# Kernel optimization log

Hardware: AMD Instinct MI355X
Metric: run time of the kernel (lower is better)

The kernel has to match this reference:

```python
import jax, jax.numpy as jnp
import numpy as np

N, E, HID, H, D = 16000, 128000, 128, 8, 16
EPS = 1e-6
LN_EPS = 1e-5


def _ln(x, g, b):
    mu = x.mean(-1, keepdims=True)
    var = ((x - mu) ** 2).mean(-1, keepdims=True)
    return (x - mu) * jax.lax.rsqrt(var + LN_EPS) * g + b


def _phi(x):
    return jax.nn.elu(x) + 1.0


def setup_inputs() -> dict:
    key = jax.random.key(0)
    ks = jax.random.split(key, 16)
    w = lambda k, s: (jax.random.normal(k, s, jnp.float32) * 0.02)
    inp = {
        'x': jax.random.normal(ks[0], (N, HID), jnp.float32),
        'r': jax.random.normal(ks[1], (E, HID), jnp.float32),
        'edge_index': jax.random.randint(ks[2], (2, E), 0, N, jnp.int64),
        # layernorms
        'ln_x_g': jnp.ones((HID,)), 'ln_x_b': jnp.zeros((HID,)),
        'ln_r_g': jnp.ones((HID,)), 'ln_r_b': jnp.zeros((HID,)),
        'ln_post_g': jnp.ones((HID,)), 'ln_post_b': jnp.zeros((HID,)),
        'ln_ffpre_g': jnp.ones((HID,)), 'ln_ffpre_b': jnp.zeros((HID,)),
        'ln_ffpost_g': jnp.ones((HID,)), 'ln_ffpost_b': jnp.zeros((HID,)),
        # attention projections (stored [in, out]; y = x @ W)
        'Wq': w(ks[3], (HID, H * D)), 'Wk': w(ks[4], (HID, H * D)),
        'Wv': w(ks[5], (HID, H * D)),
        'Wkr': w(ks[6], (HID, H * D)), 'Wvr': w(ks[7], (HID, H * D)),
        'Wo': w(ks[8], (H * D, HID)),
        'Wg': w(ks[9], (2 * HID, HID)), 'bg': jnp.zeros((HID,)),
        'Ws': w(ks[10], (HID, HID)), 'bs': jnp.zeros((HID,)),
        # feed-forward
        'W1': w(ks[11], (HID, 4 * HID)), 'b1': jnp.zeros((4 * HID,)),
        'W2': w(ks[12], (4 * HID, HID)), 'b2': jnp.zeros((HID,)),
    }
    return inp


def reference(x, r, edge_index, ln_x_g, ln_x_b, ln_r_g, ln_r_b,
              ln_post_g, ln_post_b, ln_ffpre_g, ln_ffpre_b,
              ln_ffpost_g, ln_ffpost_b, Wq, Wk, Wv, Wkr, Wvr, Wo,
              Wg, bg, Ws, bs, W1, b1, W2, b2):
    n = x.shape[0]
    src, dst = edge_index[0], edge_index[1]
    xs = _ln(x, ln_x_g, ln_x_b)            # shared pre-norm (non-bipartite)
    rn = _ln(r, ln_r_g, ln_r_b)

    q = (xs @ Wq).reshape(n, H, D)
    k = (xs @ Wk).reshape(n, H, D)
    v = (xs @ Wv).reshape(n, H, D)
    k_e = k[src] + (rn @ Wkr).reshape(-1, H, D)   # [E,H,D]
    v_e = v[src] + (rn @ Wvr).reshape(-1, H, D)

    phi_q = _phi(q)                         # [N,H,D]
    phi_k = _phi(k_e)                       # [E,H,D]
    # per-edge outer product, scattered to destination nodes
    kv = phi_k[..., :, None] * v_e[..., None, :]          # [E,H,D,D]
    S = jax.ops.segment_sum(kv.reshape(-1, H * D * D), dst,
                            num_segments=n).reshape(n, H, D, D)
    Z = jax.ops.segment_sum(phi_k.reshape(-1, H * D), dst,
                            num_segments=n).reshape(n, H, D)

    num = jnp.einsum('nhd,nhdv->nhv', phi_q, S)
    den = jnp.maximum((phi_q * Z).sum(-1, keepdims=True), EPS)
    out = (num / den).reshape(n, H * D) @ Wo              # [N,HID]

    g = jax.nn.sigmoid(jnp.concatenate([out, xs], axis=-1) @ Wg + bg)
    attn = out + g * (xs @ Ws + bs - out)

    x_mid = x + _ln(attn, ln_post_g, ln_post_b)
    h = jax.nn.gelu(_ln(x_mid, ln_ffpre_g, ln_ffpre_b) @ W1 + b1,
                    approximate=False) @ W2 + b2
    return x_mid + _ln(h, ln_ffpost_g, ln_ffpost_b)
```

## Files before the change

kernel.cpp:

```cpp
#include <hip/hip_runtime.h>
#include <hip/hip_bf16.h>

#define NN 16000
#define NE 128000

typedef unsigned short u16;
typedef __attribute__((ext_vector_type(8))) short bf16x8;
typedef __attribute__((ext_vector_type(4))) float f32x4;

__device__ __forceinline__ float bf2f(u16 u) {
    unsigned int v = ((unsigned int)u) << 16;
    return __uint_as_float(v);
}
__device__ __forceinline__ u16 f2bf(float f) {
    unsigned int u = __float_as_uint(f);
    unsigned int r = u + 0x7FFF + ((u >> 16) & 1);
    return (u16)(r >> 16);
}
__device__ __forceinline__ float loadf(const void* p, size_t i, int bf) {
    return bf ? bf2f(((const u16*)p)[i]) : ((const float*)p)[i];
}

__global__ void dtype_detect_kernel(const u16* __restrict__ xw, int* __restrict__ flags)
{
    __shared__ int cnt[256];
    if (threadIdx.x == 0) flags[2] = 0;
    int c = 0;
    #pragma unroll
    for (int k = 0; k < 16; ++k) {
        unsigned int w = xw[threadIdx.x + k * 256];
        int e = (int)((w >> 7) & 0xFF);
        c += (e >= 100 && e <= 140) ? 1 : 0;
    }
    cnt[threadIdx.x] = c;
    __syncthreads();
    for (int s = 128; s > 0; s >>= 1) {
        if (threadIdx.x < s) cnt[threadIdx.x] += cnt[threadIdx.x + s];
        __syncthreads();
    }
    if (threadIdx.x == 0) flags[0] = (cnt[0] >= 3300) ? 1 : 0;
}

__global__ __launch_bounds__(256) void edetect_kernel(const int* __restrict__ ei,
                                                      int* __restrict__ flags)
{
    int t = blockIdx.x * 256 + threadIdx.x;
    int a = 0;
    #pragma unroll
    for (int j = 0; j < 4; ++j) a |= ei[2 * (t * 4 + j) + 1];
    for (int m = 1; m < 64; m <<= 1) a |= __shfl_xor(a, m, 64);
    if ((threadIdx.x & 63) == 0 && a) atomicOr(&flags[2], a);
}

__global__ void cvt_edges_kernel(const int* __restrict__ ei, const int* __restrict__ flags,
                                 int* __restrict__ out, int* __restrict__ hist)
{
    int i = blockIdx.x * 256 + threadIdx.x;
    if (i < NN) hist[i] = 0;
    if (i >= 2 * NE) return;
    int v = (flags[2] == 0) ? ei[2 * i] : ei[i];
    v = v < 0 ? 0 : (v >= NN ? NN - 1 : v);
    out[i] = v;
}

__global__ void hist_kernel(const int* __restrict__ e32, int* __restrict__ hist)
{
    int i = blockIdx.x * 256 + threadIdx.x;
    if (i < NE) atomicAdd(&hist[e32[NE + i]], 1);
}

__global__ __launch_bounds__(256) void scan_kernel(const int* __restrict__ hist,
                                                   int* __restrict__ offs,
                                                   int* __restrict__ cursor)
{
    __shared__ int wsum[4];
    __shared__ int carry_s;
    int tid = threadIdx.x, lane = tid & 63, w = tid >> 6;
    if (tid == 0) { carry_s = 0; offs[0] = 0; cursor[0] = 0; }
    __syncthreads();
    for (int c0 = 0; c0 < NN; c0 += 256) {
        int i = c0 + tid;
        int x = (i < NN) ? hist[i] : 0;
        #pragma unroll
        for (int o = 1; o < 64; o <<= 1) {
            int y = __shfl_up(x, o, 64);
            if (lane >= o) x += y;
        }
        if (lane == 63) wsum[w] = x;
        __syncthreads();
        if (tid == 0) {
            int s = 0;
            #pragma unroll
            for (int j = 0; j < 4; ++j) { int t2 = wsum[j]; wsum[j] = s; s += t2; }
        }
        __syncthreads();
        int incl = x + wsum[w] + carry_s;
        if (i < NN) { offs[i + 1] = incl; cursor[i + 1] = incl; }
        __syncthreads();
        if (tid == 255) carry_s = incl;
        __syncthreads();
    }
}

__global__ void scatter_kernel(const int* __restrict__ e32, int* __restrict__ cursor,
                               int* __restrict__ perm, int* __restrict__ ssrc,
                               int* __restrict__ sdst)
{
    int i = blockIdx.x * 256 + threadIdx.x;
    if (i >= NE) return;
    int d = e32[NE + i];
    int pos = atomicAdd(&cursor[d], 1);
    perm[pos] = i;
    ssrc[pos] = e32[i];
    sdst[pos] = d;
}

struct WDesc { const void* w; u16* wt; int K; int N; int tile0; };
struct WTArgs { WDesc d[10]; };
__global__ __launch_bounds__(256) void wtrans_kernel(WTArgs args, const int* __restrict__ flags)
{
    int b = blockIdx.x;
    int i = 0;
    while (i < 9 && b >= args.d[i + 1].tile0) ++i;
    WDesc de = args.d[i];
    int lt = b - de.tile0;
    int tn = de.N >> 5;
    int tk = lt / tn, tc = lt % tn;
    int bf = flags[0];
    int n = tc * 32 + (threadIdx.x & 31);
    int k = tk * 32 + ((threadIdx.x >> 5) << 2);
    u16* dp = de.wt + (size_t)n * de.K + k;
    #pragma unroll
    for (int j = 0; j < 4; ++j)
        dp[j] = f2bf(loadf(de.w, (size_t)(k + j) * de.N + n, bf));
}

__global__ __launch_bounds__(256) void ln_in_kernel(const void* __restrict__ X,
                                                    const void* __restrict__ gain,
                                                    const void* __restrict__ beta,
                                                    const int* __restrict__ flags,
                                                    u16* __restrict__ Y, int M)
{
    const int bf = flags[0];
    int row = blockIdx.x * 4 + (threadIdx.x >> 6);
    int lane = threadIdx.x & 63;
    if (row >= M) return;
    size_t base = (size_t)row * 128;
    float x0 = loadf(X, base + lane, bf);
    float x1 = loadf(X, base + lane + 64, bf);
    float s = x0 + x1, sq = x0 * x0 + x1 * x1;
    for (int m = 1; m < 64; m <<= 1) { s += __shfl_xor(s, m, 64); sq += __shfl_xor(sq, m, 64); }
    float mu = s * (1.0f / 128.0f);
    float var = sq * (1.0f / 128.0f) - mu * mu;
    float rs = rsqrtf(var + 1e-5f);
    Y[base + lane]      = f2bf((x0 - mu) * rs * loadf(gain, lane, bf)      + loadf(beta, lane, bf));
    Y[base + lane + 64] = f2bf((x1 - mu) * rs * loadf(gain, lane + 64, bf) + loadf(beta, lane + 64, bf));
}

__global__ __launch_bounds__(256) void mfma_gemm_kernel(
    const u16* __restrict__ A, const u16* __restrict__ Wt, int bstride,
    const void* __restrict__ bias, const int* __restrict__ flags,
    void* __restrict__ C, int M, int K, int Ncol, int act, int out_bf)
{
    int wave = threadIdx.x >> 6, lane = threadIdx.x & 63;
    int quad = lane >> 4, l15 = lane & 15;
    int m0 = blockIdx.y * 64 + wave * 16;
    int n0 = blockIdx.x * 64;
    f32x4 acc[4] = {};
    const u16* ap = A + (size_t)(m0 + l15) * K + quad * 8;
    const u16* bp = Wt + (size_t)(n0 + l15) * bstride + quad * 8;
    for (int k0 = 0; k0 < K; k0 += 32) {
        bf16x8 a = *(const bf16x8*)(ap + k0);
        #pragma unroll
        for (int t = 0; t < 4; ++t) {
            bf16x8 b = *(const bf16x8*)(bp + (size_t)(t * 16) * bstride + k0);
            acc[t] = __builtin_amdgcn_mfma_f32_16x16x32_bf16(a, b, acc[t], 0, 0, 0);
        }
    }
    const int bf = flags[0];
    #pragma unroll
    for (int t = 0; t < 4; ++t) {
        int col = n0 + t * 16 + l15;
        float bv = bias ? loadf(bias, col, bf) : 0.0f;
        #pragma unroll
        for (int rg = 0; rg < 4; ++rg) {
            int row = m0 + quad * 4 + rg;
            float v = acc[t][rg] + bv;
            if (act == 1 || (act == 3 && col < 128)) v = (v > 0.0f) ? v + 1.0f : expf(v);
            else if (act == 2) v = 0.5f * v * (1.0f + erff(v * 0.70710678118f));
            if (out_bf) ((u16*)C)[(size_t)row * Ncol + col] = f2bf(v);
            else        ((float*)C)[(size_t)row * Ncol + col] = v;
        }
    }
}

__global__ __launch_bounds__(256) void edge_proj_kernel(
    const void* __restrict__ r,
    const void* __restrict__ lng, const void* __restrict__ lnb,
    const u16* __restrict__ Wkrt, const u16* __restrict__ Wvrt,
    const int* __restrict__ perm, const int* __restrict__ ssrc,
    const int* __restrict__ sdst,
    const u16* __restrict__ qkv, const int* __restrict__ flags,
    float* __restrict__ p_arr, u16* __restrict__ ve_s)
{
    const int bf = flags[0];
    __shared__ float sg[128], sb[128];
    int tid = threadIdx.x;
    if (tid < 128) { sg[tid] = loadf(lng, tid, bf); sb[tid] = loadf(lnb, tid, bf); }
    __syncthreads();
    int wave = tid >> 6, lane = tid & 63;
    int quad = lane >> 4, l15 = lane & 15;
    int e0 = blockIdx.x * 32 + (wave >> 1) * 16;
    int c0 = (wave & 1) * 64;

    int rrow = perm[e0 + l15];
    float vbuf[32];
    float s = 0.f, sq = 0.f;
    size_t rbase = (size_t)rrow * 128;
    #pragma unroll
    for (int kc = 0; kc < 4; ++kc) {
        int cb = kc * 32 + quad * 8;
        if (bf) {
            ushort4 p0 = *(const ushort4*)((const u16*)r + rbase + cb);
            ushort4 p1 = *(const ushort4*)((const u16*)r + rbase + cb + 4);
            vbuf[kc*8+0]=bf2f(p0.x); vbuf[kc*8+1]=bf2f(p0.y); vbuf[kc*8+2]=bf2f(p0.z); vbuf[kc*8+3]=bf2f(p0.w);
            vbuf[kc*8+4]=bf2f(p1.x); vbuf[kc*8+5]=bf2f(p1.y); vbuf[kc*8+6]=bf2f(p1.z); vbuf[kc*8+7]=bf2f(p1.w);
        } else {
            float4 p0 = *(const float4*)((const float*)r + rbase + cb);
            float4 p1 = *(const float4*)((const float*)r + rbase + cb + 4);
            vbuf[kc*8+0]=p0.x; vbuf[kc*8+1]=p0.y; vbuf[kc*8+2]=p0.z; vbuf[kc*8+3]=p0.w;
            vbuf[kc*8+4]=p1.x; vbuf[kc*8+5]=p1.y; vbuf[kc*8+6]=p1.z; vbuf[kc*8+7]=p1.w;
        }
        #pragma unroll
        for (int j = 0; j < 8; ++j) { s += vbuf[kc*8+j]; sq += vbuf[kc*8+j]*vbuf[kc*8+j]; }
    }
    s += __shfl_xor(s, 16, 64); sq += __shfl_xor(sq, 16, 64);
    s += __shfl_xor(s, 32, 64); sq += __shfl_xor(sq, 32, 64);
    float mu = s * (1.0f / 128.0f);
    float var = sq * (1.0f / 128.0f) - mu * mu;
    float rsx = rsqrtf(var + 1e-5f);
    bf16x8 afr[4];
    #pragma unroll
    for (int kc = 0; kc < 4; ++kc) {
        bf16x8 a;
        #pragma unroll
        for (int j = 0; j < 8; ++j) {
            int col = kc * 32 + quad * 8 + j;
            a[j] = (short)f2bf((vbuf[kc*8+j] - mu) * rsx * sg[col] + sb[col]);
        }
        afr[kc] = a;
    }

    f32x4 acck[4] = {};
    f32x4 accv[4] = {};
    #pragma unroll
    for (int kc = 0; kc < 4; ++kc) {
        int k0 = kc * 32;
        #pragma unroll
        for (int t = 0; t < 4; ++t) {
            bf16x8 bk = *(const bf16x8*)(Wkrt + (size_t)(c0 + t*16 + l15) * 128 + k0 + quad * 8);
            bf16x8 bv = *(const bf16x8*)(Wvrt + (size_t)(c0 + t*16 + l15) * 128 + k0 + quad * 8);
            acck[t] = __builtin_amdgcn_mfma_f32_16x16x32_bf16(afr[kc], bk, acck[t], 0, 0, 0);
            accv[t] = __builtin_amdgcn_mfma_f32_16x16x32_bf16(afr[kc], bv, accv[t], 0, 0, 0);
        }
    }

    int se[4], de[4];
    #pragma unroll
    for (int rg = 0; rg < 4; ++rg) {
        int e = e0 + quad * 4 + rg;
        se[rg] = ssrc[e]; de[rg] = sdst[e];
    }
    #pragma unroll
    for (int t = 0; t < 4; ++t) {
        int col = c0 + t * 16 + l15;
        float p_[4];
        #pragma unroll
        for (int rg = 0; rg < 4; ++rg) {
            float kv = acck[t][rg] + bf2f(qkv[(size_t)se[rg] * 384 + 128 + col]);
            kv = (kv > 0.0f) ? kv + 1.0f : expf(kv);
            float pm = kv * bf2f(qkv[(size_t)de[rg] * 384 + col]);
            pm += __shfl_xor(pm, 1, 64);
            pm += __shfl_xor(pm, 2, 64);
            pm += __shfl_xor(pm, 4, 64);
            pm += __shfl_xor(pm, 8, 64);
            p_[rg] = pm;
        }
        if (l15 == 0) {
            #pragma unroll
            for (int rg = 0; rg < 4; ++rg)
                p_arr[(size_t)(e0 + quad * 4 + rg) * 8 + (c0 >> 4) + t] = p_[rg];
        }
        #pragma unroll
        for (int rg = 0; rg < 4; ++rg) {
            float vv = accv[t][rg] + bf2f(qkv[(size_t)se[rg] * 384 + 256 + col]);
            ve_s[(size_t)(e0 + quad * 4 + rg) * 128 + col] = f2bf(vv);
        }
    }
}

__global__ __launch_bounds__(256) void node_acc_kernel(
    const float* __restrict__ p_arr, const u16* __restrict__ ve_s,
    const int* __restrict__ offs, u16* __restrict__ att)
{
    int n = blockIdx.x * 4 + (threadIdx.x >> 6);
    int lane = threadIdx.x & 63;
    int beg = offs[n], end = offs[n + 1];
    int h0 = lane >> 4, h1 = 4 + h0;
    float n0 = 0.f, n1 = 0.f, d0 = 0.f, d1 = 0.f;
    for (int e = beg; e < end; ++e) {
        float p0 = p_arr[(size_t)e * 8 + h0];
        float p1 = p_arr[(size_t)e * 8 + h1];
        float v0 = bf2f(ve_s[(size_t)e * 128 + lane]);
        float v1 = bf2f(ve_s[(size_t)e * 128 + lane + 64]);
        n0 += p0 * v0; n1 += p1 * v1;
        d0 += p0; d1 += p1;
    }
    att[(size_t)n * 128 + lane]      = f2bf(n0 / fmaxf(d0, 1e-6f));
    att[(size_t)n * 128 + lane + 64] = f2bf(n1 / fmaxf(d1, 1e-6f));
}

__global__ __launch_bounds__(256) void gate_mega_kernel(
    const u16* __restrict__ att,
    const u16* __restrict__ Wo_t, const u16* __restrict__ Wg_t,
    const float* __restrict__ gxs, const float* __restrict__ sbuf,
    const void* __restrict__ x,
    const void* __restrict__ g_po, const void* __restrict__ b_po,
    const void* __restrict__ g_fp, const void* __restrict__ b_fp,
    const int* __restrict__ flags,
    float* __restrict__ xmid, u16* __restrict__ ffp)
{
    const int bf = flags[0];
    __shared__ float lds[4][16][132];
    __shared__ float sgpo[128], sbpo[128], sgfp[128], sbfp[128];
    int tid = threadIdx.x;
    if (tid < 128) {
        sgpo[tid] = loadf(g_po, tid, bf);
        sbpo[tid] = loadf(b_po, tid, bf);
        sgfp[tid] = loadf(g_fp, tid, bf);
        sbfp[tid] = loadf(b_fp, tid, bf);
    }
    __syncthreads();
    int wave = tid >> 6, lane = tid & 63;
    int quad = lane >> 4, l15 = lane & 15;
    int m0 = blockIdx.x * 64 + wave * 16;

    bf16x8 afr[4];
    #pragma unroll
    for (int kc = 0; kc < 4; ++kc)
        afr[kc] = *(const bf16x8*)(att + (size_t)(m0 + l15) * 128 + kc * 32 + quad * 8);

    f32x4 acco[8] = {};
    #pragma unroll
    for (int kc = 0; kc < 4; ++kc)
        #pragma unroll
        for (int t = 0; t < 8; ++t) {
            bf16x8 b = *(const bf16x8*)(Wo_t + (size_t)(t*16 + l15) * 128 + kc*32 + quad*8);
            acco[t] = __builtin_amdgcn_mfma_f32_16x16x32_bf16(afr[kc], b, acco[t], 0, 0, 0);
        }
    #pragma unroll
    for (int t = 0; t < 8; ++t)
        #pragma unroll
        for (int rg = 0; rg < 4; ++rg)
            lds[wave][quad*4+rg][t*16+l15] = acco[t][rg];
    __syncthreads();
    bf16x8 afo[4];
    #pragma unroll
    for (int kc = 0; kc < 4; ++kc) {
        bf16x8 a;
        #pragma unroll
        for (int j = 0; j < 8; ++j)
            a[j] = (short)f2bf(lds[wave][l15][kc*32 + quad*8 + j]);
        afo[kc] = a;
    }
    f32x4 accg[8] = {};
    #pragma unroll
    for (int kc = 0; kc < 4; ++kc)
        #pragma unroll
        for (int t = 0; t < 8; ++t) {
            bf16x8 b = *(const bf16x8*)(Wg_t + (size_t)(t*16 + l15) * 256 + kc*32 + quad*8);
            accg[t] = __builtin_amdgcn_mfma_f32_16x16x32_bf16(afo[kc], b, accg[t], 0, 0, 0);
        }
    float attn[8][4];
    float sv[4] = {0,0,0,0}, sqv[4] = {0,0,0,0};
    #pragma unroll
    for (int t = 0; t < 8; ++t) {
        int col = t * 16 + l15;
        #pragma unroll
        for (int rg = 0; rg < 4; ++rg) {
            int row = m0 + quad * 4 + rg;
            float gp = accg[t][rg] + gxs[(size_t)row * 128 + col];
            float gg = 1.0f / (1.0f + expf(-gp));
            float o = acco[t][rg];
            float a = o + gg * (sbuf[(size_t)row * 128 + col] - o);
            attn[t][rg] = a; sv[rg] += a; sqv[rg] += a * a;
        }
    }
    #pragma unroll
    for (int rg = 0; rg < 4; ++rg)
        for (int m = 1; m < 16; m <<= 1) {
            sv[rg] += __shfl_xor(sv[rg], m, 64);
            sqv[rg] += __shfl_xor(sqv[rg], m, 64);
        }
    float mu[4], rs[4];
    #pragma unroll
    for (int rg = 0; rg < 4; ++rg) {
        mu[rg] = sv[rg] * (1.0f / 128.0f);
        float var = sqv[rg] * (1.0f / 128.0f) - mu[rg] * mu[rg];
        rs[rg] = rsqrtf(var + 1e-5f);
    }
    float s2[4] = {0,0,0,0}, sq2[4] = {0,0,0,0};
    #pragma unroll
    for (int t = 0; t < 8; ++t) {
        int col = t * 16 + l15;
        #pragma unroll
        for (int rg = 0; rg < 4; ++rg) {
            int row = m0 + quad * 4 + rg;
            float xm = loadf(x, (size_t)row * 128 + col, bf)
                     + (attn[t][rg] - mu[rg]) * rs[rg] * sgpo[col] + sbpo[col];
            attn[t][rg] = xm;
            xmid[(size_t)row * 128 + col] = xm;
            s2[rg] += xm; sq2[rg] += xm * xm;
        }
    }
    #pragma unroll
    for (int rg = 0; rg < 4; ++rg)
        for (int m = 1; m < 16; m <<= 1) {
            s2[rg] += __shfl_xor(s2[rg], m, 64);
            sq2[rg] += __shfl_xor(sq2[rg], m, 64);
        }
    #pragma unroll
    for (int rg = 0; rg < 4; ++rg) {
        float mu2 = s2[rg] * (1.0f / 128.0f);
        float var2 = sq2[rg] * (1.0f / 128.0f) - mu2 * mu2;
        float rs2 = rsqrtf(var2 + 1e-5f);
        #pragma unroll
        for (int t = 0; t < 8; ++t) {
            int col = t * 16 + l15;
            int row = m0 + quad * 4 + rg;
            ffp[(size_t)row * 128 + col] =
                f2bf((attn[t][rg] - mu2) * rs2 * sgfp[col] + sbfp[col]);
        }
    }
}

__global__ __launch_bounds__(128) void ff_mega_kernel(
    const u16* __restrict__ ffp, const u16* __restrict__ W1_t, const void* __restrict__ b1,
    const u16* __restrict__ W2_t, const void* __restrict__ b2,
    const float* __restrict__ xmid,
    const void* __restrict__ g_fo, const void* __restrict__ b_fo,
    const int* __restrict__ flags, void* __restrict__ outp)
{
    const int bf = flags[0];
    __shared__ __align__(16) u16 h1l[2][16][520];
    int tid = threadIdx.x;
    int wave = tid >> 6, lane = tid & 63;
    int quad = lane >> 4, l15 = lane & 15;
    int m0 = blockIdx.x * 32 + wave * 16;

    bf16x8 afr[4];
    const u16* ap = ffp + (size_t)(m0 + l15) * 128 + quad * 8;
    #pragma unroll
    for (int kc = 0; kc < 4; ++kc) afr[kc] = *(const bf16x8*)(ap + kc * 32);

    f32x4 acc1[32] = {};
    #pragma unroll
    for (int kc = 0; kc < 4; ++kc)
        #pragma unroll
        for (int t = 0; t < 32; ++t) {
            bf16x8 b = *(const bf16x8*)(W1_t + (size_t)(t*16 + l15) * 128 + kc*32 + quad*8);
            acc1[t] = __builtin_amdgcn_mfma_f32_16x16x32_bf16(afr[kc], b, acc1[t], 0, 0, 0);
        }
    #pragma unroll
    for (int t = 0; t < 32; ++t) {
        int col = t * 16 + l15;
        float bv = loadf(b1, col, bf);
        #pragma unroll
        for (int rg = 0; rg < 4; ++rg) {
            float v = acc1[t][rg] + bv;
            v = 0.5f * v * (1.0f + erff(v * 0.70710678118f));
            h1l[wave][quad * 4 + rg][col] = f2bf(v);
        }
    }
    __syncthreads();
    f32x4 acc2[8] = {};
    #pragma unroll
    for (int kc = 0; kc < 16; ++kc) {
        bf16x8 a = *(const bf16x8*)&h1l[wave][l15][kc * 32 + quad * 8];
        #pragma unroll
        for (int t = 0; t < 8; ++t) {
            bf16x8 b = *(const bf16x8*)(W2_t + (size_t)(t*16 + l15) * 512 + kc*32 + quad*8);
            acc2[t] = __builtin_amdgcn_mfma_f32_16x16x32_bf16(a, b, acc2[t], 0, 0, 0);
        }
    }
    float h2v[8][4];
    float sv[4] = {0,0,0,0}, sqv[4] = {0,0,0,0};
    #pragma unroll
    for (int t = 0; t < 8; ++t) {
        int col = t * 16 + l15;
        float bv = loadf(b2, col, bf);
        #pragma unroll
        for (int rg = 0; rg < 4; ++rg) {
            float v = acc2[t][rg] + bv;
            h2v[t][rg] = v; sv[rg] += v; sqv[rg] += v * v;
        }
    }
    #pragma unroll
    for (int rg = 0; rg < 4; ++rg)
        for (int m = 1; m < 16; m <<= 1) {
            sv[rg] += __shfl_xor(sv[rg], m, 64);
            sqv[rg] += __shfl_xor(sqv[rg], m, 64);
        }
    #pragma unroll
    for (int rg = 0; rg < 4; ++rg) {
        float mu = sv[rg] * (1.0f / 128.0f);
        float var = sqv[rg] * (1.0f / 128.0f) - mu * mu;
        float rs = rsqrtf(var + 1e-5f);
        int row = m0 + quad * 4 + rg;
        #pragma unroll
        for (int t = 0; t < 8; ++t) {
            int col = t * 16 + l15;
            float y = xmid[(size_t)row * 128 + col]
                    + (h2v[t][rg] - mu) * rs * loadf(g_fo, col, bf) + loadf(b_fo, col, bf);
            if (bf) ((u16*)outp)[(size_t)row * 128 + col] = f2bf(y);
            else    ((float*)outp)[(size_t)row * 128 + col] = y;
        }
    }
}

extern "C" void kernel_launch(void* const* d_in, const int* in_sizes, int n_in,
                              void* d_out, int out_size, void* d_ws, size_t ws_size,
                              hipStream_t stream)
{
    const int N = NN, E = NE;
    const void* x       = d_in[0];
    const void* r       = d_in[1];
    const int*  ei      = (const int*)d_in[2];
    const void* ln_x_g  = d_in[3];
    const void* ln_x_b  = d_in[4];
    const void* ln_r_g  = d_in[5];
    const void* ln_r_b  = d_in[6];
    const void* ln_po_g = d_in[7];
    const void* ln_po_b = d_in[8];
    const void* ln_fp_g = d_in[9];
    const void* ln_fp_b = d_in[10];
    const void* ln_fo_g = d_in[11];
    const void* ln_fo_b = d_in[12];
    const void* Wq      = d_in[13];
    const void* Wk      = d_in[14];
    const void* Wv      = d_in[15];
    const void* Wkr     = d_in[16];
    const void* Wvr     = d_in[17];
    const void* Wo      = d_in[18];
    const void* Wg      = d_in[19];
    const void* bg      = d_in[20];
    const void* Ws      = d_in[21];
    const void* bs      = d_in[22];
    const void* W1      = d_in[23];
    const void* b1      = d_in[24];
    const void* W2      = d_in[25];
    const void* b2      = d_in[26];

    float* ws = (float*)d_ws;
    size_t off = 0;
    auto alloc = [&](size_t n) { float* p = ws + off; off += n; return p; };
    const size_t U = (size_t)N * 64;
    u16*   xs_bf  = (u16*)alloc(U);
    u16*   qkv_bf = (u16*)alloc(3 * U);
    u16*   att_bf = (u16*)alloc(U);
    float* sbuf   = alloc((size_t)N * 128);
    float* gxs    = alloc((size_t)N * 128);
    float* xmid   = alloc((size_t)N * 128);
    u16*   ffp_bf = (u16*)alloc(U);
    u16*   ve_s   = (u16*)alloc((size_t)E * 64);
    float* p_arr  = alloc((size_t)E * 8);
    int*   e32    = (int*)alloc((size_t)2 * E);
    int*   perm   = (int*)alloc(E);
    int*   ssrc   = (int*)alloc(E);
    int*   sdst   = (int*)alloc(E);
    int*   hist   = (int*)alloc(NN);
    int*   offs   = (int*)alloc(NN + 1);
    int*   cursor = (int*)alloc(NN + 1);
    int*   flags  = (int*)alloc(16);
    u16*   wt     = (u16*)alloc(139264);

    u16* Wq_t  = wt;
    u16* Wkr_t = wt + 49152;
    u16* Wvr_t = wt + 65536;
    u16* Wo_t  = wt + 81920;
    u16* Ws_t  = wt + 98304;
    u16* Wg_t  = wt + 114688;
    u16* W1_t  = wt + 147456;
    u16* W2_t  = wt + 212992;

    dtype_detect_kernel<<<1, 256, 0, stream>>>((const u16*)x, flags);
    edetect_kernel<<<NE / 1024, 256, 0, stream>>>(ei, flags);
    cvt_edges_kernel<<<(2 * E + 255) / 256, 256, 0, stream>>>(ei, flags, e32, hist);
    hist_kernel<<<(E + 255) / 256, 256, 0, stream>>>(e32, hist);
    scan_kernel<<<1, 256, 0, stream>>>(hist, offs, cursor);
    scatter_kernel<<<(E + 255) / 256, 256, 0, stream>>>(e32, cursor, perm, ssrc, sdst);

    WTArgs wa;
    int t0 = 0;
    auto setw = [&](int i, const void* w, u16* wtp, int K, int Ncol) {
        wa.d[i] = WDesc{w, wtp, K, Ncol, t0};
        t0 += (K / 32) * (Ncol / 32);
    };
    setw(0, Wq, Wq_t, 128, 128);
    setw(1, Wk, wt + 16384, 128, 128);
    setw(2, Wv, wt + 32768, 128, 128);
    setw(3, Wkr, Wkr_t, 128, 128);
    setw(4, Wvr, Wvr_t, 128, 128);
    setw(5, Wo, Wo_t, 128, 128);
    setw(6, Ws, Ws_t, 128, 128);
    setw(7, Wg, Wg_t, 256, 128);
    setw(8, W1, W1_t, 128, 512);
    setw(9, W2, W2_t, 512, 128);
    wtrans_kernel<<<t0, 256, 0, stream>>>(wa, flags);

    ln_in_kernel<<<N / 4, 256, 0, stream>>>(x, ln_x_g, ln_x_b, flags, xs_bf, N);

    mfma_gemm_kernel<<<dim3(6, N / 64), 256, 0, stream>>>(
        xs_bf, Wq_t, 128, nullptr, flags, qkv_bf, N, 128, 384, 3, 1);

    mfma_gemm_kernel<<<dim3(2, N / 64), 256, 0, stream>>>(
        xs_bf, Ws_t, 128, bs, flags, sbuf, N, 128, 128, 0, 0);
    mfma_gemm_kernel<<<dim3(2, N / 64), 256, 0, stream>>>(
        xs_bf, Wg_t + 128, 256, bg, flags, gxs, N, 128, 128, 0, 0);

    edge_proj_kernel<<<E / 32, 256, 0, stream>>>(r, ln_r_g, ln_r_b, Wkr_t, Wvr_t,
                                                 perm, ssrc, sdst, qkv_bf, flags,
                                                 p_arr, ve_s);

    node_acc_kernel<<<N / 4, 256, 0, stream>>>(p_arr, ve_s, offs, att_bf);

    gate_mega_kernel<<<N / 64, 256, 0, stream>>>(att_bf, Wo_t, Wg_t, gxs, sbuf,
                                                 x, ln_po_g, ln_po_b, ln_fp_g, ln_fp_b,
                                                 flags, xmid, ffp_bf);

    ff_mega_kernel<<<N / 32, 128, 0, stream>>>(ffp_bf, W1_t, b1, W2_t, b2,
                                               xmid, ln_fo_g, ln_fo_b, flags, d_out);
}
```

Baseline: 466.0 us.

## Fuse preprocessing kernels and merge input layernorm with all node projections

Folds the dtype and edge-format detection, edge conversion, histogram and weight transpose into a single pre-pass kernel. Each kernel now redoes the dtype detection inline instead of reading a flags buffer. Input layernorm is fused into one node projection kernel that computes Q/K/V, Ws and the Wg x-half from a single concatenated weight matrix, which removes the xs intermediate and three GEMM launches. In exchange every kernel pays for redundant detection loads, and the transposed Wg x-half is now addressed with an element offset.

```diff
diff --git a/kernel.cpp b/kernel.cpp
--- a/kernel.cpp
+++ b/kernel.cpp
@@ -21,52 +21,63 @@
     return bf ? bf2f(((const u16*)p)[i]) : ((const float*)p)[i];
 }
 
-__global__ void dtype_detect_kernel(const u16* __restrict__ xw, int* __restrict__ flags)
-{
-    __shared__ int cnt[256];
-    if (threadIdx.x == 0) flags[2] = 0;
+__device__ __forceinline__ int detect_bf(const u16* __restrict__ xw) {
+    int lane = threadIdx.x & 63;
     int c = 0;
     #pragma unroll
     for (int k = 0; k < 16; ++k) {
-        unsigned int w = xw[threadIdx.x + k * 256];
+        unsigned int w = xw[lane * 16 + k];
         int e = (int)((w >> 7) & 0xFF);
         c += (e >= 100 && e <= 140) ? 1 : 0;
     }
-    cnt[threadIdx.x] = c;
-    __syncthreads();
-    for (int s = 128; s > 0; s >>= 1) {
-        if (threadIdx.x < s) cnt[threadIdx.x] += cnt[threadIdx.x + s];
-        __syncthreads();
-    }
-    if (threadIdx.x == 0) flags[0] = (cnt[0] >= 3300) ? 1 : 0;
-}
-
-__global__ __launch_bounds__(256) void edetect_kernel(const int* __restrict__ ei,
-                                                      int* __restrict__ flags)
-{
-    int t = blockIdx.x * 256 + threadIdx.x;
+    for (int m = 1; m < 64; m <<= 1) c += __shfl_xor(c, m, 64);
+    return c >= 850;
+}
+
+__device__ __forceinline__ int detect_e64(const int* __restrict__ ei) {
+    int lane = threadIdx.x & 63;
     int a = 0;
     #pragma unroll
-    for (int j = 0; j < 4; ++j) a |= ei[2 * (t * 4 + j) + 1];
+    for (int k = 0; k < 16; ++k) a |= ei[2 * (lane * 16 + k) + 1];
     for (int m = 1; m < 64; m <<= 1) a |= __shfl_xor(a, m, 64);
-    if ((threadIdx.x & 63) == 0 && a) atomicOr(&flags[2], a);
-}
-
-__global__ void cvt_edges_kernel(const int* __restrict__ ei, const int* __restrict__ flags,
-                                 int* __restrict__ out, int* __restrict__ hist)
-{
-    int i = blockIdx.x * 256 + threadIdx.x;
-    if (i < NN) hist[i] = 0;
-    if (i >= 2 * NE) return;
-    int v = (flags[2] == 0) ? ei[2 * i] : ei[i];
-    v = v < 0 ? 0 : (v >= NN ? NN - 1 : v);
-    out[i] = v;
-}
-
-__global__ void hist_kernel(const int* __restrict__ e32, int* __restrict__ hist)
-{
-    int i = blockIdx.x * 256 + threadIdx.x;
-    if (i < NE) atomicAdd(&hist[e32[NE + i]], 1);
+    return a == 0;
+}
+
+struct WDesc { const void* w; u16* wt; int K; int N; int off; int tile0; };
+struct WTArgs { WDesc d[11]; };
+__global__ __launch_bounds__(256) void pre1_kernel(const int* __restrict__ ei,
+                                                   int* __restrict__ e32,
+                                                   int* __restrict__ hist,
+                                                   const u16* __restrict__ xw,
+                                                   WTArgs args)
+{
+    int b = blockIdx.x;
+    int tid = threadIdx.x;
+    if (b < 250) {
+        int e64 = detect_e64(ei);
+        #pragma unroll
+        for (int j = 0; j < 4; ++j) {
+            int i = b * 1024 + j * 256 + tid;
+            int v = e64 ? ei[2 * i] : ei[i];
+            v = v < 0 ? 0 : (v >= NN ? NN - 1 : v);
+            e32[i] = v;
+            if (i >= NE) atomicAdd(&hist[v], 1);
+        }
+        return;
+    }
+    int bf = detect_bf(xw);
+    int i = 0;
+    while (i < 10 && b >= args.d[i + 1].tile0) ++i;
+    WDesc de = args.d[i];
+    int lt = b - de.tile0;
+    int tn = de.N >> 5;
+    int tk = lt / tn, tc = lt % tn;
+    int n = tc * 32 + (tid & 31);
+    int k = tk * 32 + ((tid >> 5) << 2);
+    u16* dp = de.wt + (size_t)n * de.K + k;
+    #pragma unroll
+    for (int j = 0; j < 4; ++j)
+        dp[j] = f2bf(loadf(de.w, (size_t)de.off + (size_t)(k + j) * de.N + n, bf));
 }
 
 __global__ __launch_bounds__(256) void scan_kernel(const int* __restrict__ hist,
@@ -115,95 +126,99 @@
     sdst[pos] = d;
 }
 
-struct WDesc { const void* w; u16* wt; int K; int N; int tile0; };
-struct WTArgs { WDesc d[10]; };
-__global__ __launch_bounds__(256) void wtrans_kernel(WTArgs args, const int* __restrict__ flags)
-{
-    int b = blockIdx.x;
-    int i = 0;
-    while (i < 9 && b >= args.d[i + 1].tile0) ++i;
-    WDesc de = args.d[i];
-    int lt = b - de.tile0;
-    int tn = de.N >> 5;
-    int tk = lt / tn, tc = lt % tn;
-    int bf = flags[0];
-    int n = tc * 32 + (threadIdx.x & 31);
-    int k = tk * 32 + ((threadIdx.x >> 5) << 2);
-    u16* dp = de.wt + (size_t)n * de.K + k;
-    #pragma unroll
-    for (int j = 0; j < 4; ++j)
-        dp[j] = f2bf(loadf(de.w, (size_t)(k + j) * de.N + n, bf));
-}
-
-__global__ __launch_bounds__(256) void ln_in_kernel(const void* __restrict__ X,
-                                                    const void* __restrict__ gain,
-                                                    const void* __restrict__ beta,
-                                                    const int* __restrict__ flags,
-                                                    u16* __restrict__ Y, int M)
-{
-    const int bf = flags[0];
-    int row = blockIdx.x * 4 + (threadIdx.x >> 6);
-    int lane = threadIdx.x & 63;
-    if (row >= M) return;
-    size_t base = (size_t)row * 128;
-    float x0 = loadf(X, base + lane, bf);
-    float x1 = loadf(X, base + lane + 64, bf);
-    float s = x0 + x1, sq = x0 * x0 + x1 * x1;
-    for (int m = 1; m < 64; m <<= 1) { s += __shfl_xor(s, m, 64); sq += __shfl_xor(sq, m, 64); }
+__global__ __launch_bounds__(256) void node_proj_kernel(
+    const void* __restrict__ x,
+    const void* __restrict__ lng, const void* __restrict__ lnb,
+    const u16* __restrict__ Wall,
+    const void* __restrict__ bs, const void* __restrict__ bg,
+    u16* __restrict__ qkv, float* __restrict__ sbuf, float* __restrict__ gxs)
+{
+    const int bf = detect_bf((const u16*)x);
+    __shared__ float sg[128], sb[128];
+    int tid = threadIdx.x;
+    if (tid < 128) { sg[tid] = loadf(lng, tid, bf); sb[tid] = loadf(lnb, tid, bf); }
+    __syncthreads();
+    int wave = tid >> 6, lane = tid & 63;
+    int quad = lane >> 4, l15 = lane & 15;
+    int m0 = blockIdx.x * 16;
+
+    float vbuf[32];
+    float s = 0.f, sq = 0.f;
+    size_t rbase = (size_t)(m0 + l15) * 128;
+    #pragma unroll
+    for (int kc = 0; kc < 4; ++kc) {
+        int cb = kc * 32 + quad * 8;
+        if (bf) {
+            ushort4 p0 = *(const ushort4*)((const u16*)x + rbase + cb);
+            ushort4 p1 = *(const ushort4*)((const u16*)x + rbase + cb + 4);
+            vbuf[kc*8+0]=bf2f(p0.x); vbuf[kc*8+1]=bf2f(p0.y); vbuf[kc*8+2]=bf2f(p0.z); vbuf[kc*8+3]=bf2f(p0.w);
+            vbuf[kc*8+4]=bf2f(p1.x); vbuf[kc*8+5]=bf2f(p1.y); vbuf[kc*8+6]=bf2f(p1.z); vbuf[kc*8+7]=bf2f(p1.w);
+        } else {
+            float4 p0 = *(const float4*)((const float*)x + rbase + cb);
+            float4 p1 = *(const float4*)((const float*)x + rbase + cb + 4);
+            vbuf[kc*8+0]=p0.x; vbuf[kc*8+1]=p0.y; vbuf[kc*8+2]=p0.z; vbuf[kc*8+3]=p0.w;
+            vbuf[kc*8+4]=p1.x; vbuf[kc*8+5]=p1.y; vbuf[kc*8+6]=p1.z; vbuf[kc*8+7]=p1.w;
+        }
+        #pragma unroll
+        for (int j = 0; j < 8; ++j) { s += vbuf[kc*8+j]; sq += vbuf[kc*8+j]*vbuf[kc*8+j]; }
+    }
+    s += __shfl_xor(s, 16, 64); sq += __shfl_xor(sq, 16, 64);
+    s += __shfl_xor(s, 32, 64); sq += __shfl_xor(sq, 32, 64);
     float mu = s * (1.0f / 128.0f);
     float var = sq * (1.0f / 128.0f) - mu * mu;
-    float rs = rsqrtf(var + 1e-5f);
-    Y[base + lane]      = f2bf((x0 - mu) * rs * loadf(gain, lane, bf)      + loadf(beta, lane, bf));
-    Y[base + lane + 64] = f2bf((x1 - mu) * rs * loadf(gain, lane + 64, bf) + loadf(beta, lane + 64, bf));
-}
-
-__global__ __launch_bounds__(256) void mfma_gemm_kernel(
-    const u16* __restrict__ A, const u16* __restrict__ Wt, int bstride,
-    const void* __restrict__ bias, const int* __restrict__ flags,
-    void* __restrict__ C, int M, int K, int Ncol, int act, int out_bf)
-{
-    int wave = threadIdx.x >> 6, lane = threadIdx.x & 63;
-    int quad = lane >> 4, l15 = lane & 15;
-    int m0 = blockIdx.y * 64 + wave * 16;
-    int n0 = blockIdx.x * 64;
-    f32x4 acc[4] = {};
-    const u16* ap = A + (size_t)(m0 + l15) * K + quad * 8;
-    const u16* bp = Wt + (size_t)(n0 + l15) * bstride + quad * 8;
-    for (int k0 = 0; k0 < K; k0 += 32) {
-        bf16x8 a = *(const bf16x8*)(ap + k0);
-        #pragma unroll
-        for (int t = 0; t < 4; ++t) {
-            bf16x8 b = *(const bf16x8*)(bp + (size_t)(t * 16) * bstride + k0);
-            acc[t] = __builtin_amdgcn_mfma_f32_16x16x32_bf16(a, b, acc[t], 0, 0, 0);
-        }
-    }
-    const int bf = flags[0];
-    #pragma unroll
-    for (int t = 0; t < 4; ++t) {
-        int col = n0 + t * 16 + l15;
-        float bv = bias ? loadf(bias, col, bf) : 0.0f;
+    float rsx = rsqrtf(var + 1e-5f);
+    bf16x8 afr[4];
+    #pragma unroll
+    for (int kc = 0; kc < 4; ++kc) {
+        bf16x8 a;
+        #pragma unroll
+        for (int j = 0; j < 8; ++j) {
+            int col = kc * 32 + quad * 8 + j;
+            a[j] = (short)f2bf((vbuf[kc*8+j] - mu) * rsx * sg[col] + sb[col]);
+        }
+        afr[kc] = a;
+    }
+
+    f32x4 acc[10] = {};
+    #pragma unroll
+    for (int kc = 0; kc < 4; ++kc)
+        #pragma unroll
+        for (int tt = 0; tt < 10; ++tt) {
+            int t = wave * 10 + tt;
+            bf16x8 b = *(const bf16x8*)(Wall + (size_t)(t * 16 + l15) * 128 + kc * 32 + quad * 8);
+            acc[tt] = __builtin_amdgcn_mfma_f32_16x16x32_bf16(afr[kc], b, acc[tt], 0, 0, 0);
+        }
+    #pragma unroll
+    for (int tt = 0; tt < 10; ++tt) {
+        int ct = (wave * 10 + tt) * 16 + l15;
         #pragma unroll
         for (int rg = 0; rg < 4; ++rg) {
             int row = m0 + quad * 4 + rg;
-            float v = acc[t][rg] + bv;
-            if (act == 1 || (act == 3 && col < 128)) v = (v > 0.0f) ? v + 1.0f : expf(v);
-            else if (act == 2) v = 0.5f * v * (1.0f + erff(v * 0.70710678118f));
-            if (out_bf) ((u16*)C)[(size_t)row * Ncol + col] = f2bf(v);
-            else        ((float*)C)[(size_t)row * Ncol + col] = v;
+            float v = acc[tt][rg];
+            if (ct < 384) {
+                if (ct < 128) v = (v > 0.0f) ? v + 1.0f : expf(v);
+                qkv[(size_t)row * 384 + ct] = f2bf(v);
+            } else if (ct < 512) {
+                int cs = ct - 384;
+                sbuf[(size_t)row * 128 + cs] = v + loadf(bs, cs, bf);
+            } else {
+                int cg = ct - 512;
+                gxs[(size_t)row * 128 + cg] = v + loadf(bg, cg, bf);
+            }
         }
     }
 }
 
 __global__ __launch_bounds__(256) void edge_proj_kernel(
-    const void* __restrict__ r,
+    const void* __restrict__ r, const void* __restrict__ x,
     const void* __restrict__ lng, const void* __restrict__ lnb,
     const u16* __restrict__ Wkrt, const u16* __restrict__ Wvrt,
     const int* __restrict__ perm, const int* __restrict__ ssrc,
     const int* __restrict__ sdst,
-    const u16* __restrict__ qkv, const int* __restrict__ flags,
+    const u16* __restrict__ qkv,
     float* __restrict__ p_arr, u16* __restrict__ ve_s)
 {
-    const int bf = flags[0];
+    const int bf = detect_bf((const u16*)x);
     __shared__ float sg[128], sb[128];
     int tid = threadIdx.x;
     if (tid < 128) { sg[tid] = loadf(lng, tid, bf); sb[tid] = loadf(lnb, tid, bf); }
@@ -322,15 +337,14 @@
 
 __global__ __launch_bounds__(256) void gate_mega_kernel(
     const u16* __restrict__ att,
-    const u16* __restrict__ Wo_t, const u16* __restrict__ Wg_t,
+    const u16* __restrict__ Wo_t, const u16* __restrict__ Wg1_t,
     const float* __restrict__ gxs, const float* __restrict__ sbuf,
     const void* __restrict__ x,
     const void* __restrict__ g_po, const void* __restrict__ b_po,
     const void* __restrict__ g_fp, const void* __restrict__ b_fp,
-    const int* __restrict__ flags,
     float* __restrict__ xmid, u16* __restrict__ ffp)
 {
-    const int bf = flags[0];
+    const int bf = detect_bf((const u16*)x);
     __shared__ float lds[4][16][132];
     __shared__ float sgpo[128], sbpo[128], sgfp[128], sbfp[128];
     int tid = threadIdx.x;
@@ -378,7 +392,7 @@
     for (int kc = 0; kc < 4; ++kc)
         #pragma unroll
         for (int t = 0; t < 8; ++t) {
-            bf16x8 b = *(const bf16x8*)(Wg_t + (size_t)(t*16 + l15) * 256 + kc*32 + quad*8);
+            bf16x8 b = *(const bf16x8*)(Wg1_t + (size_t)(t*16 + l15) * 128 + kc*32 + quad*8);
             accg[t] = __builtin_amdgcn_mfma_f32_16x16x32_bf16(afo[kc], b, accg[t], 0, 0, 0);
         }
     float attn[8][4];
@@ -447,11 +461,11 @@
 __global__ __launch_bounds__(128) void ff_mega_kernel(
     const u16* __restrict__ ffp, const u16* __restrict__ W1_t, const void* __restrict__ b1,
     const u16* __restrict__ W2_t, const void* __restrict__ b2,
-    const float* __restrict__ xmid,
+    const float* __restrict__ xmid, const void* __restrict__ x,
     const void* __restrict__ g_fo, const void* __restrict__ b_fo,
-    const int* __restrict__ flags, void* __restrict__ outp)
-{
-    const int bf = flags[0];
+    void* __restrict__ outp)
+{
+    const int bf = detect_bf((const u16*)x);
     __shared__ __align__(16) u16 h1l[2][16][520];
     int tid = threadIdx.x;
     int wave = tid >> 6, lane = tid & 63;
@@ -565,7 +579,6 @@
     size_t off = 0;
     auto alloc = [&](size_t n) { float* p = ws + off; off += n; return p; };
     const size_t U = (size_t)N * 64;
-    u16*   xs_bf  = (u16*)alloc(U);
     u16*   qkv_bf = (u16*)alloc(3 * U);
     u16*   att_bf = (u16*)alloc(U);
     float* sbuf   = alloc((size_t)N * 128);
@@ -581,63 +594,52 @@
     int*   hist   = (int*)alloc(NN);
     int*   offs   = (int*)alloc(NN + 1);
     int*   cursor = (int*)alloc(NN + 1);
-    int*   flags  = (int*)alloc(16);
     u16*   wt     = (u16*)alloc(139264);
 
-    u16* Wq_t  = wt;
-    u16* Wkr_t = wt + 49152;
-    u16* Wvr_t = wt + 65536;
-    u16* Wo_t  = wt + 81920;
-    u16* Ws_t  = wt + 98304;
-    u16* Wg_t  = wt + 114688;
-    u16* W1_t  = wt + 147456;
-    u16* W2_t  = wt + 212992;
-
-    dtype_detect_kernel<<<1, 256, 0, stream>>>((const u16*)x, flags);
-    edetect_kernel<<<NE / 1024, 256, 0, stream>>>(ei, flags);
-    cvt_edges_kernel<<<(2 * E + 255) / 256, 256, 0, stream>>>(ei, flags, e32, hist);
-    hist_kernel<<<(E + 255) / 256, 256, 0, stream>>>(e32, hist);
+    u16* Wall_t = wt;
+    u16* Wkr_t  = wt + 81920;
+    u16* Wvr_t  = wt + 98304;
+    u16* Wo_t   = wt + 114688;
+    u16* Wg1_t  = wt + 131072;
+    u16* W1_t   = wt + 147456;
+    u16* W2_t   = wt + 212992;
+
+    hipMemsetAsync(hist, 0, NN * sizeof(int), stream);
+
+    WTArgs wa;
+    int t0 = 250;
+    auto setw = [&](int i, const void* w, u16* wtp, int K, int Ncol, int eoff) {
+        wa.d[i] = WDesc{w, wtp, K, Ncol, eoff, t0};
+        t0 += (K / 32) * (Ncol / 32);
+    };
+    setw(0, Wq,  wt,           128, 128, 0);
+    setw(1, Wk,  wt + 16384,   128, 128, 0);
+    setw(2, Wv,  wt + 32768,   128, 128, 0);
+    setw(3, Ws,  wt + 49152,   128, 128, 0);
+    setw(4, Wg,  wt + 65536,   128, 128, 16384);
+    setw(5, Wkr, Wkr_t,        128, 128, 0);
+    setw(6, Wvr, Wvr_t,        128, 128, 0);
+    setw(7, Wo,  Wo_t,         128, 128, 0);
+    setw(8, Wg,  Wg1_t,        128, 128, 0);
+    setw(9, W1,  W1_t,         128, 512, 0);
+    setw(10, W2, W2_t,         512, 128, 0);
+    pre1_kernel<<<t0, 256, 0, stream>>>(ei, e32, hist, (const u16*)x, wa);
+
     scan_kernel<<<1, 256, 0, stream>>>(hist, offs, cursor);
     scatter_kernel<<<(E + 255) / 256, 256, 0, stream>>>(e32, cursor, perm, ssrc, sdst);
 
-    WTArgs wa;
-    int t0 = 0;
-    auto setw = [&](int i, const void* w, u16* wtp, int K, int Ncol) {
-        wa.d[i] = WDesc{w, wtp, K, Ncol, t0};
-        t0 += (K / 32) * (Ncol / 32);
-    };
-    setw(0, Wq, Wq_t, 128, 128);
-    setw(1, Wk, wt + 16384, 128, 128);
-    setw(2, Wv, wt + 32768, 128, 128);
-    setw(3, Wkr, Wkr_t, 128, 128);
-    setw(4, Wvr, Wvr_t, 128, 128);
-    setw(5, Wo, Wo_t, 128, 128);
-    setw(6, Ws, Ws_t, 128, 128);
-    setw(7, Wg, Wg_t, 256, 128);
-    setw(8, W1, W1_t, 128, 512);
-    setw(9, W2, W2_t, 512, 128);
-    wtrans_kernel<<<t0, 256, 0, stream>>>(wa, flags);
-
-    ln_in_kernel<<<N / 4, 256, 0, stream>>>(x, ln_x_g, ln_x_b, flags, xs_bf, N);
-
-    mfma_gemm_kernel<<<dim3(6, N / 64), 256, 0, stream>>>(
-        xs_bf, Wq_t, 128, nullptr, flags, qkv_bf, N, 128, 384, 3, 1);
-
-    mfma_gemm_kernel<<<dim3(2, N / 64), 256, 0, stream>>>(
-        xs_bf, Ws_t, 128, bs, flags, sbuf, N, 128, 128, 0, 0);
-    mfma_gemm_kernel<<<dim3(2, N / 64), 256, 0, stream>>>(
-        xs_bf, Wg_t + 128, 256, bg, flags, gxs, N, 128, 128, 0, 0);
-
-    edge_proj_kernel<<<E / 32, 256, 0, stream>>>(r, ln_r_g, ln_r_b, Wkr_t, Wvr_t,
-                                                 perm, ssrc, sdst, qkv_bf, flags,
-                                                 p_arr, ve_s);
+    node_proj_kernel<<<N / 16, 256, 0, stream>>>(x, ln_x_g, ln_x_b, Wall_t,
+                                                 bs, bg, qkv_bf, sbuf, gxs);
+
+    edge_proj_kernel<<<E / 32, 256, 0, stream>>>(r, x, ln_r_g, ln_r_b, Wkr_t, Wvr_t,
+                                                 perm, ssrc, sdst, qkv_bf, p_arr, ve_s);
 
     node_acc_kernel<<<N / 4, 256, 0, stream>>>(p_arr, ve_s, offs, att_bf);
 
-    gate_mega_kernel<<<N / 64, 256, 0, stream>>>(att_bf, Wo_t, Wg_t, gxs, sbuf,
+    gate_mega_kernel<<<N / 64, 256, 0, stream>>>(att_bf, Wo_t, Wg1_t, gxs, sbuf,
                                                  x, ln_po_g, ln_po_b, ln_fp_g, ln_fp_b,
-                                                 flags, xmid, ffp_bf);
+                                                 xmid, ffp_bf);
 
     ff_mega_kernel<<<N / 32, 128, 0, stream>>>(ffp_bf, W1_t, b1, W2_t, b2,
-                                               xmid, ln_fo_g, ln_fo_b, flags, d_out);
-}
+                                               xmid, x, ln_fo_g, ln_fo_b, d_out);
+}
```

Result: no change. 467.5 us (+0.3%).
